# Kernel optimization log

Hardware: AMD Instinct MI355X
Metric: run time of the kernel (lower is better)

The kernel has to match this reference:

```python
import jax, jax.numpy as jnp
import numpy as np

HIDDEN = 1024
N_HEADS = 16
N_KV = 4
HEAD_DIM = HIDDEN // N_HEADS  # 64


def setup_inputs() -> dict:
    key = jax.random.key(0)
    ks = jax.random.split(key, 10)
    B, S, D = 2, 2048, HIDDEN
    s = 0.02
    return {
        "hidden_states": jax.random.normal(ks[0], (B, S, D), jnp.float32),
        "attention_mask": jnp.ones((B, S), jnp.float32),
        "Wq": jax.random.normal(ks[1], (D, N_HEADS * HEAD_DIM), jnp.float32) * s,
        "bq": jnp.zeros((N_HEADS * HEAD_DIM,), jnp.float32),
        "Wk": jax.random.normal(ks[2], (D, N_KV * HEAD_DIM), jnp.float32) * s,
        "bk": jnp.zeros((N_KV * HEAD_DIM,), jnp.float32),
        "Wv": jax.random.normal(ks[3], (D, N_KV * HEAD_DIM), jnp.float32) * s,
        "bv": jnp.zeros((N_KV * HEAD_DIM,), jnp.float32),
        "Wo": jax.random.normal(ks[4], (D, D), jnp.float32) * s,
        "bo": jnp.zeros((D,), jnp.float32),
    }


def _rope(x):
    # x: [B, H, S, Dh]; half-split RoPE as in the torch module
    S, Dh = x.shape[-2], x.shape[-1]
    inv_freq = 1.0 / (10000.0 ** (jnp.arange(0, Dh, 2, dtype=jnp.float32) / Dh))
    freqs = jnp.arange(S, dtype=jnp.float32)[:, None] * inv_freq[None, :]  # [S, Dh/2]
    cos, sin = jnp.cos(freqs), jnp.sin(freqs)
    x1, x2 = jnp.split(x, 2, axis=-1)
    return jnp.concatenate([x1 * cos - x2 * sin, x1 * sin + x2 * cos], axis=-1)


def reference(hidden_states, attention_mask, Wq, bq, Wk, bk, Wv, bv, Wo, bo):
    B, S, D = hidden_states.shape
    q = (hidden_states @ Wq + bq).reshape(B, S, N_HEADS, HEAD_DIM).transpose(0, 2, 1, 3)
    k = (hidden_states @ Wk + bk).reshape(B, S, N_KV, HEAD_DIM).transpose(0, 2, 1, 3)
    v = (hidden_states @ Wv + bv).reshape(B, S, N_KV, HEAD_DIM).transpose(0, 2, 1, 3)
    q = _rope(q)
    k = _rope(k)
    rep = N_HEADS // N_KV
    k = jnp.repeat(k, rep, axis=1)  # [B, H, S, Dh]
    v = jnp.repeat(v, rep, axis=1)
    bias = (1.0 - attention_mask[:, None, None, :]) * -1e9  # [B,1,1,S]
    scores = jnp.einsum("bhqd,bhkd->bhqk", q, k) / jnp.sqrt(jnp.float32(HEAD_DIM))
    attn = jax.nn.softmax(scores + bias, axis=-1)
    out = jnp.einsum("bhqk,bhkd->bhqd", attn, v)
    out = out.transpose(0, 2, 1, 3).reshape(B, S, D)
    return out @ Wo + bo
```

## Files before the change

### kernel.cpp

```cpp
#include <hip/hip_runtime.h>

typedef __bf16 bf16;
typedef __attribute__((ext_vector_type(8))) __bf16 bf16x8;
typedef __attribute__((ext_vector_type(4))) __bf16 bf16x4;
typedef __attribute__((ext_vector_type(4))) float f32x4;

#define LOG2E 1.44269504088896340736f
#define QSCALE 0.18033688011112042f

__device__ inline void tr_tile(const float* __restrict__ in, bf16* __restrict__ out,
                               int R, int C, int bx, int by, int tid) {
    __shared__ float t[32][33];
    int tx = tid & 31, ty = tid >> 5;
    int rbase = by * 32, cbase = bx * 32;
#pragma unroll
    for (int i = 0; i < 4; i++) {
        int r = ty + i * 8;
        t[r][tx] = in[(size_t)(rbase + r) * C + cbase + tx];
    }
    __syncthreads();
#pragma unroll
    for (int i = 0; i < 4; i++) {
        int r = ty + i * 8;
        out[(size_t)(cbase + r) * R + rbase + tx] = (bf16)t[tx][r];
    }
}

__global__ __launch_bounds__(256) void prep_k(const float* __restrict__ X,
                                              const float* __restrict__ Wq,
                                              const float* __restrict__ Wk,
                                              const float* __restrict__ Wv,
                                              const float* __restrict__ Wo,
                                              const float* __restrict__ mask,
                                              bf16* __restrict__ Xb,
                                              bf16* __restrict__ WqT,
                                              bf16* __restrict__ WkT,
                                              bf16* __restrict__ WvT,
                                              bf16* __restrict__ WoT,
                                              float2* __restrict__ rt,
                                              float* __restrict__ Mb,
                                              int* __restrict__ mflags) {
    int blk = blockIdx.x, tid = threadIdx.x;
    if (blk < 2048) {
        int idx = (blk * 256 + tid) * 8;
        float4 a = *(const float4*)(X + idx);
        float4 b = *(const float4*)(X + idx + 4);
        bf16 v[8] = {(bf16)a.x, (bf16)a.y, (bf16)a.z, (bf16)a.w,
                     (bf16)b.x, (bf16)b.y, (bf16)b.z, (bf16)b.w};
        *(uint4*)(Xb + idx) = *(const uint4*)v;
    } else if (blk < 3072) {
        int t = blk - 2048; tr_tile(Wq, WqT, 1024, 1024, t & 31, t >> 5, tid);
    } else if (blk < 3328) {
        int t = blk - 3072; tr_tile(Wk, WkT, 1024, 256, t & 7, t >> 3, tid);
    } else if (blk < 3584) {
        int t = blk - 3328; tr_tile(Wv, WvT, 1024, 256, t & 7, t >> 3, tid);
    } else if (blk < 4608) {
        int t = blk - 3584; tr_tile(Wo, WoT, 1024, 1024, t & 31, t >> 5, tid);
    } else if (blk < 4864) {
        int idx = (blk - 4608) * 256 + tid;
        int s = idx >> 5, i = idx & 31;
        float inv = exp2f(-0.41524100370589830f * (float)i);
        float ang = (float)s * inv;
        rt[idx] = make_float2(cosf(ang), sinf(ang));
    } else {
        __shared__ int sflag;
        int b = blk - 4864;
        if (tid == 0) sflag = 1;
        __syncthreads();
        const float* mrow = mask + (size_t)b * 2048;
        int i0 = tid * 8;
        bool ones = true;
#pragma unroll
        for (int j = 0; j < 8; j++) {
            float m = mrow[i0 + j];
            if (m != 1.0f) ones = false;
            Mb[(size_t)b * 2048 + i0 + j] = (1.0f - m) * (-1e9f) * LOG2E;
        }
        if (!ones) sflag = 0;
        __syncthreads();
        if (tid == 0) mflags[b] = sflag;
    }
}

__global__ __launch_bounds__(256) void vtrans_k(const unsigned short* __restrict__ in,
                                                unsigned short* __restrict__ out) {
    __shared__ unsigned short t[32][33];
    int z = blockIdx.z;
    const unsigned short* ip = in + (size_t)z * 2048 * 64;
    unsigned short* op = out + (size_t)z * 2048 * 64;
    int tx = threadIdx.x & 31, ty = threadIdx.x >> 5;
    int rbase = blockIdx.y * 32, cbase = blockIdx.x * 32;
#pragma unroll
    for (int i = 0; i < 4; i++) {
        int r = ty + i * 8;
        t[r][tx] = ip[(size_t)(rbase + r) * 64 + cbase + tx];
    }
    __syncthreads();
#pragma unroll
    for (int i = 0; i < 4; i++) {
        int r = ty + i * 8;
        op[(size_t)(cbase + r) * 2048 + rbase + tx] = t[tx][r];
    }
}

__device__ __forceinline__ void gemm_main_12864(const bf16* __restrict__ A,
                                                const bf16* __restrict__ BT,
                                                int m0, int n0, int tid,
                                                f32x4 (&acc)[2][4]) {
    __shared__ bf16 As[128 * 64];
    __shared__ bf16 Bs[64 * 64];
    int w = tid >> 6, lane = tid & 63, l15 = lane & 15, quad = lane >> 4;

    int srow = lane >> 3;
    int kx = ((lane & 7) ^ srow) * 8;
    const bf16* ga0 = A + (size_t)(m0 + w * 32 + srow) * 1024 + kx;
    const bf16* gb0 = BT + (size_t)(n0 + w * 16 + srow) * 1024 + kx;
    bf16* la0 = As + (w * 32) * 64 + lane * 8;
    bf16* lb0 = Bs + (w * 16) * 64 + lane * 8;

    for (int k0 = 0; k0 < 1024; k0 += 64) {
#pragma unroll
        for (int p = 0; p < 4; p++)
            __builtin_amdgcn_global_load_lds(
                (const __attribute__((address_space(1))) unsigned int*)(ga0 + (size_t)p * 8 * 1024 + k0),
                (__attribute__((address_space(3))) unsigned int*)(la0 + p * 512), 16, 0, 0);
#pragma unroll
        for (int p = 0; p < 2; p++)
            __builtin_amdgcn_global_load_lds(
                (const __attribute__((address_space(1))) unsigned int*)(gb0 + (size_t)p * 8 * 1024 + k0),
                (__attribute__((address_space(3))) unsigned int*)(lb0 + p * 512), 16, 0, 0);
        __syncthreads();
#pragma unroll
        for (int half = 0; half < 2; half++) {
            bf16x8 a[2], bfr[4];
            int kp = ((half * 4 + quad) ^ (l15 & 7)) * 8;
#pragma unroll
            for (int i = 0; i < 2; i++)
                a[i] = *(const bf16x8*)&As[(w * 32 + i * 16 + l15) * 64 + kp];
#pragma unroll
            for (int j = 0; j < 4; j++)
                bfr[j] = *(const bf16x8*)&Bs[(j * 16 + l15) * 64 + kp];
#pragma unroll
            for (int i = 0; i < 2; i++)
#pragma unroll
                for (int j = 0; j < 4; j++)
                    acc[i][j] = __builtin_amdgcn_mfma_f32_16x16x32_bf16(a[i], bfr[j], acc[i][j], 0, 0, 0);
        }
        __syncthreads();
    }
}

__global__ __launch_bounds__(256) void qkv_gemm2(const bf16* __restrict__ Xb,
                                                 const bf16* __restrict__ WTall,
                                                 const float* __restrict__ bq,
                                                 const float* __restrict__ bk,
                                                 const float* __restrict__ bv,
                                                 const float2* __restrict__ rt,
                                                 bf16* __restrict__ Qb,
                                                 bf16* __restrict__ Kb,
                                                 bf16* __restrict__ Vb) {
    int tt = blockIdx.x, gy = blockIdx.y, tid = threadIdx.x;
    f32x4 acc[2][4] = {};
    gemm_main_12864(Xb, WTall, tt * 128, gy * 64, tid, acc);

    int w = tid >> 6, lane = tid & 63, l15 = lane & 15, quad = lane >> 4;
    const float* bias;
    bf16* dst;
    int mode, head;
    if (gy < 16)      { head = gy;      bias = bq + head * 64; dst = Qb; mode = 0; }
    else if (gy < 20) { head = gy - 16; bias = bk + head * 64; dst = Kb; mode = 1; }
    else              { head = gy - 20; bias = bv + head * 64; dst = Vb; mode = 2; }

#pragma unroll
    for (int i = 0; i < 2; i++) {
#pragma unroll
        for (int r = 0; r < 4; r++) {
            int token = tt * 128 + w * 32 + i * 16 + quad * 4 + r;
            int b = token >> 11, s = token & 2047;
            float vals[4];
#pragma unroll
            for (int j = 0; j < 4; j++) vals[j] = acc[i][j][r] + bias[j * 16 + l15];
            if (mode <= 1) {
#pragma unroll
                for (int c = 0; c < 2; c++) {
                    float2 cs2 = rt[s * 32 + c * 16 + l15];
                    float x1 = vals[c], x2 = vals[c + 2];
                    vals[c]     = x1 * cs2.x - x2 * cs2.y;
                    vals[c + 2] = x1 * cs2.y + x2 * cs2.x;
                }
            }
            if (mode == 0) {
#pragma unroll
                for (int j = 0; j < 4; j++) vals[j] *= QSCALE;
            }
            size_t base;
            if (mode == 0) base = (((size_t)b * 16 + head) * 2048 + s) * 64;
            else           base = (((size_t)b * 4  + head) * 2048 + s) * 64;
#pragma unroll
            for (int j = 0; j < 4; j++) dst[base + j * 16 + l15] = (bf16)vals[j];
        }
    }
}

__global__ __launch_bounds__(256) void oproj_gemm2(const bf16* __restrict__ Ab,
                                                   const bf16* __restrict__ WoT,
                                                   const float* __restrict__ bo,
                                                   float* __restrict__ out) {
    int tt = blockIdx.x, nt = blockIdx.y, tid = threadIdx.x;
    f32x4 acc[2][4] = {};
    gemm_main_12864(Ab, WoT, tt * 128, nt * 64, tid, acc);

    int w = tid >> 6, lane = tid & 63, l15 = lane & 15, quad = lane >> 4;
#pragma unroll
    for (int i = 0; i < 2; i++) {
#pragma unroll
        for (int r = 0; r < 4; r++) {
            int token = tt * 128 + w * 32 + i * 16 + quad * 4 + r;
#pragma unroll
            for (int j = 0; j < 4; j++) {
                int n = nt * 64 + j * 16 + l15;
                out[(size_t)token * 1024 + n] = acc[i][j][r] + bo[n];
            }
        }
    }
}

__global__ __launch_bounds__(256) void attn_k(const bf16* __restrict__ Qb,
                                              const bf16* __restrict__ Kb,
                                              const bf16* __restrict__ VbT,
                                              const float* __restrict__ Mb,
                                              const int* __restrict__ mflags,
                                              bf16* __restrict__ Opb,
                                              float* __restrict__ Lp) {
    int qt = blockIdx.x, h = blockIdx.y, z = blockIdx.z;
    int b = z >> 1, sp = z & 1;
    int kvh = h >> 2;
    int kt0 = sp * 16;

    __shared__ bf16 Ks[2][64 * 64];
    __shared__ bf16 Vs[2][64 * 64];
    __shared__ unsigned short Ps[4][32 * 72];

    int tid = threadIdx.x, w = tid >> 6, lane = tid & 63, l15 = lane & 15, quad = lane >> 4;

    const bool maskOnes = (mflags[b] != 0);

    bf16x8 qa[2][2];
#pragma unroll
    for (int g = 0; g < 2; g++) {
        size_t qbase = (((size_t)b * 16 + h) * 2048 + (size_t)qt * 128 + w * 32 + g * 16 + l15) * 64;
        qa[g][0] = *(const bf16x8*)(Qb + qbase + quad * 8);
        qa[g][1] = *(const bf16x8*)(Qb + qbase + 32 + quad * 8);
    }

    f32x4 oacc[2][4] = {};
    f32x4 sacc[2] = {};

    bf16 one_ = (bf16)1.0f;
    bf16x8 vones = {one_, one_, one_, one_, one_, one_, one_, one_};

    size_t kRow = ((size_t)b * 4 + kvh) * 2048;
    size_t vRow = ((size_t)b * 4 + kvh) * 64;
    const float* mrow = Mb + (size_t)b * 2048 + quad * 4;

    int srow = (lane >> 3);
    int kx = ((lane & 7) ^ srow) * 8;
    const bf16* gk0 = Kb + (kRow + w * 16 + srow) * 64 + kx;
    const bf16* gv0 = VbT + (vRow + w * 16 + srow) * 2048 + kx;
    int lofs = (w * 16) * 64 + lane * 8;

#define STAGE(KT, BUF)                                                                              \
    do {                                                                                            \
        _Pragma("unroll")                                                                           \
        for (int p = 0; p < 2; p++) {                                                               \
            __builtin_amdgcn_global_load_lds(                                                       \
                (const __attribute__((address_space(1))) unsigned int*)(gk0 + ((size_t)(KT) * 64 + p * 8) * 64), \
                (__attribute__((address_space(3))) unsigned int*)(&Ks[BUF][0] + lofs + p * 512), 16, 0, 0); \
            __builtin_amdgcn_global_load_lds(                                                       \
                (const __attribute__((address_space(1))) unsigned int*)(gv0 + (size_t)p * 8 * 2048 + (KT) * 64), \
                (__attribute__((address_space(3))) unsigned int*)(&Vs[BUF][0] + lofs + p * 512), 16, 0, 0); \
        }                                                                                           \
    } while (0)

    STAGE(kt0, 0);
    __syncthreads();

    for (int kt = 0; kt < 16; kt++) {
        int cb = kt & 1;
        if (kt < 15) STAGE(kt0 + kt + 1, cb ^ 1);
        int ktg = kt0 + kt;

        const bf16* ksb = &Ks[cb][0];
        const bf16* vsb = &Vs[cb][0];

        bf16x8 ka[4][2];
#pragma unroll
        for (int c = 0; c < 4; c++) {
            int row = c * 16 + l15;
#pragma unroll
            for (int half = 0; half < 2; half++) {
                int kp = ((half * 4 + quad) ^ (l15 & 7)) * 8;
                ka[c][half] = *(const bf16x8*)&ksb[row * 64 + kp];
            }
        }

        f32x4 sc[2][4];
#pragma unroll
        for (int g = 0; g < 2; g++)
#pragma unroll
            for (int c = 0; c < 4; c++) {
                f32x4 zz = {};
                zz = __builtin_amdgcn_mfma_f32_16x16x32_bf16(ka[c][0], qa[g][0], zz, 0, 0, 0);
                zz = __builtin_amdgcn_mfma_f32_16x16x32_bf16(ka[c][1], qa[g][1], zz, 0, 0, 0);
                sc[g][c] = zz;
            }

        if (!maskOnes) {
#pragma unroll
            for (int c = 0; c < 4; c++) {
                f32x4 bias4 = *(const f32x4*)(mrow + ktg * 64 + c * 16);
#pragma unroll
                for (int r = 0; r < 4; r++) { sc[0][c][r] += bias4[r]; sc[1][c][r] += bias4[r]; }
            }
        }

#pragma unroll
        for (int g = 0; g < 2; g++) {
#pragma unroll
            for (int c = 0; c < 4; c++) {
#pragma unroll
                for (int r = 0; r < 4; r++) sc[g][c][r] = exp2f(sc[g][c][r]);
                bf16x4 pv = {(bf16)sc[g][c][0], (bf16)sc[g][c][1], (bf16)sc[g][c][2], (bf16)sc[g][c][3]};
                *(bf16x4*)&Ps[w][(g * 16 + l15) * 72 + c * 16 + quad * 4] = pv;
            }
        }

        bf16x8 vb[4][2];
#pragma unroll
        for (int c = 0; c < 4; c++) {
            int row = c * 16 + l15;
#pragma unroll
            for (int half = 0; half < 2; half++) {
                int kp = ((half * 4 + quad) ^ (l15 & 7)) * 8;
                vb[c][half] = *(const bf16x8*)&vsb[row * 64 + kp];
            }
        }
        bf16x8 pa[2][2];
#pragma unroll
        for (int g = 0; g < 2; g++) {
            pa[g][0] = *(const bf16x8*)&Ps[w][(g * 16 + l15) * 72 + quad * 8];
            pa[g][1] = *(const bf16x8*)&Ps[w][(g * 16 + l15) * 72 + 32 + quad * 8];
        }
#pragma unroll
        for (int g = 0; g < 2; g++) {
            sacc[g] = __builtin_amdgcn_mfma_f32_16x16x32_bf16(pa[g][0], vones, sacc[g], 0, 0, 0);
            sacc[g] = __builtin_amdgcn_mfma_f32_16x16x32_bf16(pa[g][1], vones, sacc[g], 0, 0, 0);
#pragma unroll
            for (int c = 0; c < 4; c++) {
                oacc[g][c] = __builtin_amdgcn_mfma_f32_16x16x32_bf16(pa[g][0], vb[c][0], oacc[g][c], 0, 0, 0);
                oacc[g][c] = __builtin_amdgcn_mfma_f32_16x16x32_bf16(pa[g][1], vb[c][1], oacc[g][c], 0, 0, 0);
            }
        }
        __syncthreads();
    }
#undef STAGE

#pragma unroll
    for (int g = 0; g < 2; g++) {
#pragma unroll
        for (int r = 0; r < 4; r++) {
            int q = qt * 128 + w * 32 + g * 16 + quad * 4 + r;
            size_t base = ((size_t)sp * 4096 + (size_t)b * 2048 + q) * 1024 + h * 64;
#pragma unroll
            for (int c = 0; c < 4; c++) Opb[base + c * 16 + l15] = (bf16)oacc[g][c][r];
        }
        if (l15 == 0) {
#pragma unroll
            for (int r = 0; r < 4; r++)
                Lp[((size_t)(sp * 2 + b) * 16 + h) * 2048 + qt * 128 + w * 32 + g * 16 + quad * 4 + r] = sacc[g][r];
        }
    }
}

__global__ __launch_bounds__(256) void merge_k(const bf16* __restrict__ Opb,
                                               const float* __restrict__ Lp,
                                               bf16* __restrict__ Ab) {
    int idx = (blockIdx.x * 256 + threadIdx.x) * 8;
    int tok = idx >> 10;
    int col = idx & 1023;
    int h = col >> 6;
    int b = tok >> 11, q = tok & 2047;
    float l0 = Lp[((size_t)b * 16 + h) * 2048 + q];
    float l1 = Lp[((size_t)(2 + b) * 16 + h) * 2048 + q];
    float inv = 1.0f / (l0 + l1);
    bf16x8 a = *(const bf16x8*)(Opb + idx);
    bf16x8 c = *(const bf16x8*)(Opb + (size_t)4096 * 1024 + idx);
    bf16 o[8];
#pragma unroll
    for (int j = 0; j < 8; j++) o[j] = (bf16)(((float)a[j] + (float)c[j]) * inv);
    *(uint4*)(Ab + idx) = *(const uint4*)o;
}

extern "C" void kernel_launch(void* const* d_in, const int* in_sizes, int n_in,
                              void* d_out, int out_size, void* d_ws, size_t ws_size,
                              hipStream_t stream) {
    const float* X    = (const float*)d_in[0];
    const float* mask = (const float*)d_in[1];
    const float* Wq   = (const float*)d_in[2];
    const float* bq   = (const float*)d_in[3];
    const float* Wk   = (const float*)d_in[4];
    const float* bk   = (const float*)d_in[5];
    const float* Wv   = (const float*)d_in[6];
    const float* bv   = (const float*)d_in[7];
    const float* Wo   = (const float*)d_in[8];
    const float* bo   = (const float*)d_in[9];
    float* out = (float*)d_out;
    bf16* ws  = (bf16*)d_ws;

    bf16* Xb  = ws;
    bf16* WqT = Xb + (size_t)4096 * 1024;
    bf16* WkT = WqT + 1024 * 1024;
    bf16* WvT = WkT + 256 * 1024;
    bf16* WoT = WvT + 256 * 1024;
    bf16* Qb  = WoT + 1024 * 1024;
    bf16* Kb  = Qb + (size_t)2 * 16 * 2048 * 64;
    bf16* Vb  = Kb + (size_t)2 * 4 * 2048 * 64;
    bf16* Ab  = Vb + (size_t)2 * 4 * 2048 * 64;
    float2* rt = (float2*)(Ab + (size_t)2 * 2048 * 1024);
    float* Mb  = (float*)(rt + 2048 * 32);
    int* mflags = (int*)(Mb + 2 * 2048);
    bf16* Opb = (bf16*)(mflags + 4);
    float* Lp = (float*)(Opb + (size_t)2 * 4096 * 1024);
    bf16* VbT = Xb;

    prep_k<<<4866, 256, 0, stream>>>(X, Wq, Wk, Wv, Wo, mask, Xb, WqT, WkT, WvT, WoT, rt, Mb, mflags);
    qkv_gemm2<<<dim3(32, 24), 256, 0, stream>>>(Xb, WqT, bq, bk, bv, rt, Qb, Kb, Vb);
    vtrans_k<<<dim3(2, 64, 8), 256, 0, stream>>>((const unsigned short*)Vb, (unsigned short*)VbT);
    attn_k<<<dim3(16, 16, 4), 256, 0, stream>>>(Qb, Kb, VbT, Mb, mflags, Opb, Lp);
    merge_k<<<2048, 256, 0, stream>>>(Opb, Lp, Ab);
    oproj_gemm2<<<dim3(32, 16), 256, 0, stream>>>(Ab, WoT, bo, out);
}
```

Baseline: 201.4 us.

## Rewrite attention inner loop with 32x32x16 MFMA and register-resident P

Switches the attention kernel from 16x16x32 to 32x32x16 bf16 MFMA tiles, computing S transposed so the exponentiated probabilities can be packed to bf16 and redistributed across lane halves with v_permlane32_swap. P then feeds the PV MFMA directly from registers instead of a round trip through shared memory. The row sum is accumulated with scalar adds plus one cross-half shuffle instead of an extra MFMA against a ones vector. Launch bounds now request 4 blocks per CU. This relies on inline gfx950 assembly and a specific MFMA register layout, and the tighter register cap could cause spills.

```diff
diff --git a/kernel.cpp b/kernel.cpp
--- a/kernel.cpp
+++ b/kernel.cpp
@@ -4,6 +4,8 @@
 typedef __attribute__((ext_vector_type(8))) __bf16 bf16x8;
 typedef __attribute__((ext_vector_type(4))) __bf16 bf16x4;
 typedef __attribute__((ext_vector_type(4))) float f32x4;
+typedef __attribute__((ext_vector_type(16))) float f32x16;
+typedef __attribute__((ext_vector_type(4))) unsigned int uint4v;
 
 #define LOG2E 1.44269504088896340736f
 #define QSCALE 0.18033688011112042f
@@ -225,13 +227,13 @@
     }
 }
 
-__global__ __launch_bounds__(256) void attn_k(const bf16* __restrict__ Qb,
-                                              const bf16* __restrict__ Kb,
-                                              const bf16* __restrict__ VbT,
-                                              const float* __restrict__ Mb,
-                                              const int* __restrict__ mflags,
-                                              bf16* __restrict__ Opb,
-                                              float* __restrict__ Lp) {
+__global__ __launch_bounds__(256, 4) void attn_k(const bf16* __restrict__ Qb,
+                                                 const bf16* __restrict__ Kb,
+                                                 const bf16* __restrict__ VbT,
+                                                 const float* __restrict__ Mb,
+                                                 const int* __restrict__ mflags,
+                                                 bf16* __restrict__ Opb,
+                                                 float* __restrict__ Lp) {
     int qt = blockIdx.x, h = blockIdx.y, z = blockIdx.z;
     int b = z >> 1, sp = z & 1;
     int kvh = h >> 2;
@@ -239,31 +241,26 @@
 
     __shared__ bf16 Ks[2][64 * 64];
     __shared__ bf16 Vs[2][64 * 64];
-    __shared__ unsigned short Ps[4][32 * 72];
-
-    int tid = threadIdx.x, w = tid >> 6, lane = tid & 63, l15 = lane & 15, quad = lane >> 4;
+
+    int tid = threadIdx.x, w = tid >> 6, lane = tid & 63, l31 = lane & 31, hi = lane >> 5;
 
     const bool maskOnes = (mflags[b] != 0);
 
-    bf16x8 qa[2][2];
-#pragma unroll
-    for (int g = 0; g < 2; g++) {
-        size_t qbase = (((size_t)b * 16 + h) * 2048 + (size_t)qt * 128 + w * 32 + g * 16 + l15) * 64;
-        qa[g][0] = *(const bf16x8*)(Qb + qbase + quad * 8);
-        qa[g][1] = *(const bf16x8*)(Qb + qbase + 32 + quad * 8);
-    }
-
-    f32x4 oacc[2][4] = {};
-    f32x4 sacc[2] = {};
-
-    bf16 one_ = (bf16)1.0f;
-    bf16x8 vones = {one_, one_, one_, one_, one_, one_, one_, one_};
+    bf16x8 qa[4];
+    {
+        size_t qrow = (((size_t)b * 16 + h) * 2048 + (size_t)qt * 128 + w * 32 + l31) * 64;
+#pragma unroll
+        for (int ds = 0; ds < 4; ds++)
+            qa[ds] = *(const bf16x8*)(Qb + qrow + ds * 16 + hi * 8);
+    }
+
+    f32x16 oacc[2] = {};
+    float lsum = 0.f;
 
     size_t kRow = ((size_t)b * 4 + kvh) * 2048;
     size_t vRow = ((size_t)b * 4 + kvh) * 64;
-    const float* mrow = Mb + (size_t)b * 2048 + quad * 4;
-
-    int srow = (lane >> 3);
+
+    int srow = lane >> 3;
     int kx = ((lane & 7) ^ srow) * 8;
     const bf16* gk0 = Kb + (kRow + w * 16 + srow) * 64 + kx;
     const bf16* gv0 = VbT + (vRow + w * 16 + srow) * 2048 + kx;
@@ -285,6 +282,8 @@
     STAGE(kt0, 0);
     __syncthreads();
 
+    const float* mbase = Mb + (size_t)b * 2048 + hi * 4;
+
     for (int kt = 0; kt < 16; kt++) {
         int cb = kt & 1;
         if (kt < 15) STAGE(kt0 + kt + 1, cb ^ 1);
@@ -293,93 +292,73 @@
         const bf16* ksb = &Ks[cb][0];
         const bf16* vsb = &Vs[cb][0];
 
-        bf16x8 ka[4][2];
-#pragma unroll
-        for (int c = 0; c < 4; c++) {
-            int row = c * 16 + l15;
-#pragma unroll
-            for (int half = 0; half < 2; half++) {
-                int kp = ((half * 4 + quad) ^ (l15 & 7)) * 8;
-                ka[c][half] = *(const bf16x8*)&ksb[row * 64 + kp];
-            }
-        }
-
-        f32x4 sc[2][4];
-#pragma unroll
-        for (int g = 0; g < 2; g++)
-#pragma unroll
-            for (int c = 0; c < 4; c++) {
-                f32x4 zz = {};
-                zz = __builtin_amdgcn_mfma_f32_16x16x32_bf16(ka[c][0], qa[g][0], zz, 0, 0, 0);
-                zz = __builtin_amdgcn_mfma_f32_16x16x32_bf16(ka[c][1], qa[g][1], zz, 0, 0, 0);
-                sc[g][c] = zz;
-            }
-
-        if (!maskOnes) {
-#pragma unroll
-            for (int c = 0; c < 4; c++) {
-                f32x4 bias4 = *(const f32x4*)(mrow + ktg * 64 + c * 16);
-#pragma unroll
-                for (int r = 0; r < 4; r++) { sc[0][c][r] += bias4[r]; sc[1][c][r] += bias4[r]; }
-            }
-        }
-
-#pragma unroll
-        for (int g = 0; g < 2; g++) {
-#pragma unroll
-            for (int c = 0; c < 4; c++) {
-#pragma unroll
-                for (int r = 0; r < 4; r++) sc[g][c][r] = exp2f(sc[g][c][r]);
-                bf16x4 pv = {(bf16)sc[g][c][0], (bf16)sc[g][c][1], (bf16)sc[g][c][2], (bf16)sc[g][c][3]};
-                *(bf16x4*)&Ps[w][(g * 16 + l15) * 72 + c * 16 + quad * 4] = pv;
-            }
-        }
-
-        bf16x8 vb[4][2];
-#pragma unroll
-        for (int c = 0; c < 4; c++) {
-            int row = c * 16 + l15;
-#pragma unroll
-            for (int half = 0; half < 2; half++) {
-                int kp = ((half * 4 + quad) ^ (l15 & 7)) * 8;
-                vb[c][half] = *(const bf16x8*)&vsb[row * 64 + kp];
-            }
-        }
-        bf16x8 pa[2][2];
-#pragma unroll
-        for (int g = 0; g < 2; g++) {
-            pa[g][0] = *(const bf16x8*)&Ps[w][(g * 16 + l15) * 72 + quad * 8];
-            pa[g][1] = *(const bf16x8*)&Ps[w][(g * 16 + l15) * 72 + 32 + quad * 8];
-        }
-#pragma unroll
-        for (int g = 0; g < 2; g++) {
-            sacc[g] = __builtin_amdgcn_mfma_f32_16x16x32_bf16(pa[g][0], vones, sacc[g], 0, 0, 0);
-            sacc[g] = __builtin_amdgcn_mfma_f32_16x16x32_bf16(pa[g][1], vones, sacc[g], 0, 0, 0);
-#pragma unroll
-            for (int c = 0; c < 4; c++) {
-                oacc[g][c] = __builtin_amdgcn_mfma_f32_16x16x32_bf16(pa[g][0], vb[c][0], oacc[g][c], 0, 0, 0);
-                oacc[g][c] = __builtin_amdgcn_mfma_f32_16x16x32_bf16(pa[g][1], vb[c][1], oacc[g][c], 0, 0, 0);
-            }
-        }
+        uint4v paw[4];
+#pragma unroll
+        for (int kh = 0; kh < 2; kh++) {
+            bf16x8 ka[4];
+#pragma unroll
+            for (int ds = 0; ds < 4; ds++) {
+                int gran = ((ds * 2 + hi) ^ (l31 & 7)) * 8;
+                ka[ds] = *(const bf16x8*)&ksb[(kh * 32 + l31) * 64 + gran];
+            }
+            f32x16 s = {};
+#pragma unroll
+            for (int ds = 0; ds < 4; ds++)
+                s = __builtin_amdgcn_mfma_f32_32x32x16_bf16(ka[ds], qa[ds], s, 0, 0, 0);
+            if (!maskOnes) {
+#pragma unroll
+                for (int g = 0; g < 4; g++) {
+                    f32x4 b4 = *(const f32x4*)(mbase + ktg * 64 + kh * 32 + g * 8);
+#pragma unroll
+                    for (int r = 0; r < 4; r++) s[g * 4 + r] += b4[r];
+                }
+            }
+#pragma unroll
+            for (int i = 0; i < 16; i++) { s[i] = exp2f(s[i]); lsum += s[i]; }
+            unsigned int d0, d1, d2, d3, d4, d5, d6, d7;
+            asm("v_cvt_pk_bf16_f32 %0, %1, %2" : "=v"(d0) : "v"(s[0]),  "v"(s[1]));
+            asm("v_cvt_pk_bf16_f32 %0, %1, %2" : "=v"(d1) : "v"(s[2]),  "v"(s[3]));
+            asm("v_cvt_pk_bf16_f32 %0, %1, %2" : "=v"(d2) : "v"(s[4]),  "v"(s[5]));
+            asm("v_cvt_pk_bf16_f32 %0, %1, %2" : "=v"(d3) : "v"(s[6]),  "v"(s[7]));
+            asm("v_cvt_pk_bf16_f32 %0, %1, %2" : "=v"(d4) : "v"(s[8]),  "v"(s[9]));
+            asm("v_cvt_pk_bf16_f32 %0, %1, %2" : "=v"(d5) : "v"(s[10]), "v"(s[11]));
+            asm("v_cvt_pk_bf16_f32 %0, %1, %2" : "=v"(d6) : "v"(s[12]), "v"(s[13]));
+            asm("v_cvt_pk_bf16_f32 %0, %1, %2" : "=v"(d7) : "v"(s[14]), "v"(s[15]));
+            asm("v_permlane32_swap_b32 %0, %1" : "+v"(d0), "+v"(d2));
+            asm("v_permlane32_swap_b32 %0, %1" : "+v"(d1), "+v"(d3));
+            asm("v_permlane32_swap_b32 %0, %1" : "+v"(d4), "+v"(d6));
+            asm("v_permlane32_swap_b32 %0, %1" : "+v"(d5), "+v"(d7));
+            paw[kh * 2 + 0][0] = d0; paw[kh * 2 + 0][1] = d1;
+            paw[kh * 2 + 0][2] = d2; paw[kh * 2 + 0][3] = d3;
+            paw[kh * 2 + 1][0] = d4; paw[kh * 2 + 1][1] = d5;
+            paw[kh * 2 + 1][2] = d6; paw[kh * 2 + 1][3] = d7;
+        }
+
+#pragma unroll
+        for (int dg = 0; dg < 2; dg++)
+#pragma unroll
+            for (int ks = 0; ks < 4; ks++) {
+                int gran = ((ks * 2 + hi) ^ (l31 & 7)) * 8;
+                bf16x8 vb = *(const bf16x8*)&vsb[(dg * 32 + l31) * 64 + gran];
+                oacc[dg] = __builtin_amdgcn_mfma_f32_32x32x16_bf16(
+                    __builtin_bit_cast(bf16x8, paw[ks]), vb, oacc[dg], 0, 0, 0);
+            }
         __syncthreads();
     }
 #undef STAGE
 
-#pragma unroll
-    for (int g = 0; g < 2; g++) {
-#pragma unroll
-        for (int r = 0; r < 4; r++) {
-            int q = qt * 128 + w * 32 + g * 16 + quad * 4 + r;
-            size_t base = ((size_t)sp * 4096 + (size_t)b * 2048 + q) * 1024 + h * 64;
-#pragma unroll
-            for (int c = 0; c < 4; c++) Opb[base + c * 16 + l15] = (bf16)oacc[g][c][r];
-        }
-        if (l15 == 0) {
-#pragma unroll
-            for (int r = 0; r < 4; r++)
-                Lp[((size_t)(sp * 2 + b) * 16 + h) * 2048 + qt * 128 + w * 32 + g * 16 + quad * 4 + r] = sacc[g][r];
-        }
-    }
+    lsum += __shfl_xor(lsum, 32, 64);
+
+#pragma unroll
+    for (int dg = 0; dg < 2; dg++)
+#pragma unroll
+        for (int reg = 0; reg < 16; reg++) {
+            int q = qt * 128 + w * 32 + (reg & 3) + 8 * (reg >> 2) + 4 * hi;
+            Opb[((size_t)sp * 4096 + (size_t)b * 2048 + q) * 1024 + h * 64 + dg * 32 + l31] =
+                (bf16)oacc[dg][reg];
+        }
+    if (hi == 0)
+        Lp[((size_t)(sp * 2 + b) * 16 + h) * 2048 + qt * 128 + w * 32 + l31] = lsum;
 }
 
 __global__ __launch_bounds__(256) void merge_k(const bf16* __restrict__ Opb,
```

Result: faster. 186.7 us (-7.3%).
